# Optimization experiments

Hardware: AMD Instinct MI355X
Metric: run time of the kernel (lower is better)

## Reference

```python
import jax, jax.numpy as jnp
import numpy as np

DIM = 128
B = 8
HM, WM = 64, 64  # target (m) spatial size


def setup_inputs() -> dict:
    key = jax.random.key(0)
    ks = jax.random.split(key, 20)
    d = DIM
    sc = 1.0 / np.sqrt(d)       # GRU / 1x1-conv fan-in scale
    sc_in = 1.0 / np.sqrt(3 * d)
    f32 = jnp.float32
    return {
        'l': jax.random.normal(ks[0], (B, d, 2 * HM, 2 * WM), f32),
        'm': jax.random.normal(ks[1], (B, d, HM, WM), f32),
        's': jax.random.normal(ks[2], (B, d, HM // 2, WM // 2), f32),
        'proj_in_w': jax.random.normal(ks[3], (d, 3 * d), f32) * sc_in,
        'proj_in_scale': jax.random.uniform(ks[4], (d,), f32, 0.5, 1.5),
        'proj_in_shift': jax.random.normal(ks[5], (d,), f32) * 0.1,
        'wih_h': jax.random.normal(ks[6], (3 * d, d), f32) * sc,
        'whh_h': jax.random.normal(ks[7], (3 * d, d), f32) * sc,
        'bih_h': jax.random.normal(ks[8], (3 * d,), f32) * 0.05,
        'bhh_h': jax.random.normal(ks[9], (3 * d,), f32) * 0.05,
        'wih_w': jax.random.normal(ks[10], (3 * d, d), f32) * sc,
        'whh_w': jax.random.normal(ks[11], (3 * d, d), f32) * sc,
        'bih_w': jax.random.normal(ks[12], (3 * d,), f32) * 0.05,
        'bhh_w': jax.random.normal(ks[13], (3 * d,), f32) * 0.05,
        'gate_w': jax.random.normal(ks[14], (d, d), f32) * sc,
        'gate_b': jax.random.normal(ks[15], (d,), f32) * 0.05,
        'proj_out_w': jax.random.normal(ks[16], (d, d), f32) * sc,
        'proj_out_scale': jax.random.uniform(ks[17], (d,), f32, 0.5, 1.5),
        'proj_out_shift': jax.random.normal(ks[18], (d,), f32) * 0.1,
    }


def _conv_bn_relu(x, w, scale, shift):
    # 1x1 conv (no bias) + folded BatchNorm (per-channel affine) + ReLU
    y = jnp.einsum('bchw,oc->bohw', x, w)
    return jax.nn.relu(y * scale[None, :, None, None] + shift[None, :, None, None])


def _gru_scan(x_seq, wih, whh, bih, bhh):
    # x_seq: [T, N, d]; PyTorch GRUCell gate layout: r | z | n
    T, N, _ = x_seq.shape
    d = whh.shape[1]
    gx = jnp.einsum('tnc,gc->tng', x_seq, wih) + bih  # input gates precomputed

    def step(h, gx_t):
        gh = h @ whh.T + bhh
        r = jax.nn.sigmoid(gx_t[:, :d] + gh[:, :d])
        z = jax.nn.sigmoid(gx_t[:, d:2 * d] + gh[:, d:2 * d])
        n = jnp.tanh(gx_t[:, 2 * d:] + r * gh[:, 2 * d:])
        h_new = (1.0 - z) * n + z * h
        return h_new, h_new

    h0 = jnp.zeros((N, d), x_seq.dtype)
    _, out = jax.lax.scan(step, h0, gx)
    return out  # [T, N, d]


def _forward(l, m, s, proj_in_w, proj_in_scale, proj_in_shift,
             wih_h, whh_h, bih_h, bhh_h, wih_w, whh_w, bih_w, bhh_w,
             gate_w, gate_b, proj_out_w, proj_out_scale, proj_out_shift):
    b, _, H, W = m.shape
    lr = jax.image.resize(l, (b, l.shape[1], H, W), 'bilinear')  # align_corners=False
    sr = jax.image.resize(s, (b, s.shape[1], H, W), 'bilinear')
    x = _conv_bn_relu(jnp.concatenate([lr, m, sr], axis=1),
                      proj_in_w, proj_in_scale, proj_in_shift)  # [b,c,H,W]
    c = x.shape[1]

    # vertical scan: sequence over H, batch (b, W)
    xh = jnp.transpose(x, (2, 0, 3, 1)).reshape(H, b * W, c)
    oh = _gru_scan(xh, wih_h, whh_h, bih_h, bhh_h).reshape(H, b, W, c)
    oh = jnp.transpose(oh, (1, 3, 0, 2))  # [b,c,H,W]

    # horizontal scan: sequence over W, batch (b, H)
    xw = jnp.transpose(x, (3, 0, 2, 1)).reshape(W, b * H, c)
    ow = _gru_scan(xw, wih_w, whh_w, bih_w, bhh_w).reshape(W, b, H, c)
    ow = jnp.transpose(ow, (1, 3, 2, 0))  # [b,c,H,W]

    scanned = oh + ow
    gate = jax.nn.sigmoid(jnp.einsum('bchw,oc->bohw', scanned, gate_w)
                          + gate_b[None, :, None, None])
    gated = scanned * gate
    return _conv_bn_relu(gated, proj_out_w, proj_out_scale, proj_out_shift) + x


def reference(l, m, s, proj_in_w, proj_in_scale, proj_in_shift,
              wih_h, whh_h, bih_h, bhh_h, wih_w, whh_w, bih_w, bhh_w,
              gate_w, gate_b, proj_out_w, proj_out_scale, proj_out_shift):
    return _forward(l, m, s, proj_in_w, proj_in_scale, proj_in_shift,
                    wih_h, whh_h, bih_h, bhh_h, wih_w, whh_w, bih_w, bhh_w,
                    gate_w, gate_b, proj_out_w, proj_out_scale, proj_out_shift)
```

## Files before the change

kernel.cpp:

```cpp
#include <hip/hip_runtime.h>


typedef __bf16 bf16;
typedef _Float16 f16;
typedef __attribute__((ext_vector_type(8))) __bf16 bf16x8;
typedef __attribute__((ext_vector_type(4))) __bf16 bf16x4;
typedef __attribute__((ext_vector_type(4))) _Float16 f16x4;
typedef __attribute__((ext_vector_type(4))) float f32x4;

__device__ __forceinline__ f32x4 mfma16(bf16x8 a, bf16x8 b, f32x4 c) {
  return __builtin_amdgcn_mfma_f32_16x16x32_bf16(a, b, c, 0, 0, 0);
}
__device__ __forceinline__ float sigm(float x) { return 1.0f / (1.0f + __expf(-x)); }
__device__ __forceinline__ float tanh_fast(float x) {
  float e = __expf(2.0f * x);
  return 1.0f - 2.0f / (e + 1.0f);
}

__global__ __launch_bounds__(256) void k_prep(
    const float* __restrict__ wpi, const float* __restrict__ wihh,
    const float* __restrict__ whhh, const float* __restrict__ wihw,
    const float* __restrict__ whhw, const float* __restrict__ wg,
    const float* __restrict__ wpo, bf16* __restrict__ dst) {
  int i = blockIdx.x * 256 + threadIdx.x;
  if (i < 49152) dst[i] = (bf16)wpi[i];
  else if (i < 98304) dst[i] = (bf16)wihh[i - 49152];
  else if (i < 147456) dst[i] = (bf16)whhh[i - 98304];
  else if (i < 196608) dst[i] = (bf16)wihw[i - 147456];
  else if (i < 245760) dst[i] = (bf16)whhw[i - 196608];
  else if (i < 262144) dst[i] = (bf16)wg[i - 245760];
  else if (i < 278528) dst[i] = (bf16)wpo[i - 262144];
}

__global__ __launch_bounds__(256, 2) void k_projin(
    const float* __restrict__ lp, const float* __restrict__ mp,
    const float* __restrict__ sp, const float* __restrict__ pscale,
    const float* __restrict__ pshift, const bf16* __restrict__ Wpi,
    f16* __restrict__ xf16, bf16* __restrict__ xb, bf16* __restrict__ xbT) {
  __shared__ __align__(16) bf16 xin[64][392];
  const int tid = threadIdx.x;
  const int bb = blockIdx.x >> 6;
  const int h = blockIdx.x & 63;

  {
    const int wq = tid & 63, cq = tid >> 6;
    float wy[4]; int iy[4];
    {
      float ssum = 0.f;
#pragma unroll
      for (int dy = 0; dy < 4; ++dy) {
        int y = 2 * h - 1 + dy;
        bool ok = (y >= 0) && (y < 128);
        iy[dy] = ok ? y : 0;
        float w0 = (dy == 0 || dy == 3) ? 0.125f : 0.375f;
        wy[dy] = ok ? w0 : 0.f;
        ssum += wy[dy];
      }
      float inv = 1.f / ssum;
#pragma unroll
      for (int dy = 0; dy < 4; ++dy) wy[dy] *= inv;
    }
    float wx[4]; int ix[4];
    {
      float ssum = 0.f;
#pragma unroll
      for (int dx = 0; dx < 4; ++dx) {
        int xq = 2 * wq - 1 + dx;
        bool ok = (xq >= 0) && (xq < 128);
        ix[dx] = ok ? xq : 0;
        float w0 = (dx == 0 || dx == 3) ? 0.125f : 0.375f;
        wx[dx] = ok ? w0 : 0.f;
        ssum += wx[dx];
      }
      float inv = 1.f / ssum;
#pragma unroll
      for (int dx = 0; dx < 4; ++dx) wx[dx] *= inv;
    }
    int syA, syB; float wsyA, wsyB;
    {
      int j0 = (h - 1) >> 1;
      float f = (h & 1) ? 0.25f : 0.75f;
      float a = 1.f - f, b2 = f;
      if (j0 < 0) a = 0.f;
      if (j0 + 1 > 31) b2 = 0.f;
      float inv = 1.f / (a + b2);
      wsyA = a * inv; wsyB = b2 * inv;
      syA = j0 < 0 ? 0 : j0;
      syB = (j0 + 1 > 31) ? 31 : (j0 + 1);
    }
    int sxA, sxB; float wsxA, wsxB;
    {
      int j0 = (wq - 1) >> 1;
      float f = (wq & 1) ? 0.25f : 0.75f;
      float a = 1.f - f, b2 = f;
      if (j0 < 0) a = 0.f;
      if (j0 + 1 > 31) b2 = 0.f;
      float inv = 1.f / (a + b2);
      wsxA = a * inv; wsxB = b2 * inv;
      sxA = j0 < 0 ? 0 : j0;
      sxB = (j0 + 1 > 31) ? 31 : (j0 + 1);
    }
    for (int ci = 0; ci < 32; ++ci) {
      int c = cq * 32 + ci;
      const float* lc = lp + ((size_t)(bb * 128 + c) << 14);
      float acc = 0.f;
#pragma unroll
      for (int dy = 0; dy < 4; ++dy) {
        const float* row = lc + (iy[dy] << 7);
        float rs = wx[0] * row[ix[0]] + wx[1] * row[ix[1]] +
                   wx[2] * row[ix[2]] + wx[3] * row[ix[3]];
        acc = fmaf(wy[dy], rs, acc);
      }
      xin[wq][c] = (bf16)acc;
      xin[wq][128 + c] = (bf16)mp[((bb * 128 + c) * 64 + h) * 64 + wq];
      const float* sc = sp + ((size_t)(bb * 128 + c) << 10);
      float sv = wsyA * (wsxA * sc[(syA << 5) + sxA] + wsxB * sc[(syA << 5) + sxB]) +
                 wsyB * (wsxA * sc[(syB << 5) + sxA] + wsxB * sc[(syB << 5) + sxB]);
      xin[wq][256 + c] = (bf16)sv;
    }
  }
  __syncthreads();

  const int lane = tid & 63, wv = tid >> 6;
  const int l16 = lane & 15, k8 = (lane >> 4) * 8, j4 = (lane >> 4) * 4;
  const f32x4 zf = {0.f, 0.f, 0.f, 0.f};
  f32x4 acc[2][4];
#pragma unroll
  for (int i = 0; i < 2; ++i)
#pragma unroll
    for (int pt = 0; pt < 4; ++pt) acc[i][pt] = zf;

  for (int kk = 0; kk < 12; ++kk) {
    bf16x8 bfr[4];
#pragma unroll
    for (int pt = 0; pt < 4; ++pt)
      bfr[pt] = *(const bf16x8*)&xin[pt * 16 + l16][kk * 32 + k8];
#pragma unroll
    for (int i = 0; i < 2; ++i) {
      bf16x8 afr = *(const bf16x8*)(Wpi + (size_t)((wv * 2 + i) * 16 + l16) * 384 + kk * 32 + k8);
#pragma unroll
      for (int pt = 0; pt < 4; ++pt) acc[i][pt] = mfma16(afr, bfr[pt], acc[i][pt]);
    }
  }
#pragma unroll
  for (int i = 0; i < 2; ++i) {
    int c0 = (wv * 2 + i) * 16 + j4;
    f32x4 scv = *(const f32x4*)&pscale[c0];
    f32x4 shv = *(const f32x4*)&pshift[c0];
#pragma unroll
    for (int pt = 0; pt < 4; ++pt) {
      int pw = pt * 16 + l16;
      bf16x4 pk;
      f16x4 pf;
#pragma unroll
      for (int j = 0; j < 4; ++j) {
        float v = fmaxf(acc[i][pt][j] * scv[j] + shv[j], 0.f);
        xf16[(size_t)((bb * 128 + c0 + j) * 64 + h) * 64 + pw] = (f16)v;
        pk[j] = (bf16)v;
        pf[j] = (f16)v;
      }
      *(bf16x4*)&xb[(size_t)(bb * 4096 + h * 64 + pw) * 128 + c0] = pk;
      *(bf16x4*)&xbT[(size_t)(bb * 4096 + pw * 64 + h) * 128 + c0] = pk;
    }
  }
}

__global__ __launch_bounds__(512, 2) void k_gx(
    const bf16* __restrict__ xb, const bf16* __restrict__ xbT,
    const bf16* __restrict__ wih_h_b, const bf16* __restrict__ wih_w_b,
    const float* __restrict__ bih_h, const float* __restrict__ bih_w,
    const float* __restrict__ bhh_h, const float* __restrict__ bhh_w,
    f16* __restrict__ gxh, f16* __restrict__ gxw) {
  const int dir = blockIdx.z;
  const int nb = blockIdx.y;
  const int t0 = blockIdx.x * 2;
  const bf16* xsrc = dir ? xbT : xb;
  const bf16* wih = dir ? wih_w_b : wih_h_b;
  const float* bih = dir ? bih_w : bih_h;
  const float* bhh = dir ? bhh_w : bhh_h;
  f16* gx = dir ? gxw : gxh;

  const int tid = threadIdx.x, lane = tid & 63, w = tid >> 6;
  const int l16 = lane & 15, k8 = (lane >> 4) * 8, j4 = (lane >> 4) * 4;
  const int n = nb * 16 + l16;
  const int pb = n >> 6, q = n & 63;

  bf16x8 afr[3][4];
#pragma unroll
  for (int part = 0; part < 3; ++part) {
    int gbase = part * 128 + w * 16;
#pragma unroll
    for (int kk = 0; kk < 4; ++kk)
      afr[part][kk] = *(const bf16x8*)(wih + (size_t)(gbase + l16) * 128 + kk * 32 + k8);
  }
  const f32x4 zf = {0.f, 0.f, 0.f, 0.f};
  f32x4 acc[3][2];
#pragma unroll
  for (int part = 0; part < 3; ++part) { acc[part][0] = zf; acc[part][1] = zf; }

#pragma unroll
  for (int pt = 0; pt < 2; ++pt) {
    const bf16* xr = xsrc + (size_t)(pb * 4096 + (t0 + pt) * 64 + q) * 128;
#pragma unroll
    for (int kk = 0; kk < 4; ++kk) {
      bf16x8 bfr = *(const bf16x8*)(xr + kk * 32 + k8);
#pragma unroll
      for (int part = 0; part < 3; ++part)
        acc[part][pt] = mfma16(afr[part][kk], bfr, acc[part][pt]);
    }
  }
#pragma unroll
  for (int part = 0; part < 3; ++part) {
    int g0 = part * 128 + w * 16 + j4;
    f32x4 bi = *(const f32x4*)&bih[g0];
    if (part < 2) {
      f32x4 bh = *(const f32x4*)&bhh[g0];
#pragma unroll
      for (int j = 0; j < 4; ++j) bi[j] += bh[j];
    }
#pragma unroll
    for (int pt = 0; pt < 2; ++pt) {
      f16x4 pk;
#pragma unroll
      for (int j = 0; j < 4; ++j) pk[j] = (f16)(acc[part][pt][j] + bi[j]);
      *(f16x4*)&gx[((size_t)(((t0 + pt) * 32 + nb) * 3 + part) * 512 + tid) * 4] = pk;
    }
  }
}

__global__ __launch_bounds__(512, 2) void k_scan(
    const bf16* __restrict__ whh_h_b, const bf16* __restrict__ whh_w_b,
    const float* __restrict__ bhh_h, const float* __restrict__ bhh_w,
    const f16* __restrict__ gxh, const f16* __restrict__ gxw,
    f16* __restrict__ ohb, f16* __restrict__ owb) {
  const int dir = blockIdx.x >> 5;
  const int nb = blockIdx.x & 31;
  const int nbase = nb * 16;
  const bf16* whh = dir ? whh_w_b : whh_h_b;
  const float* bhh = dir ? bhh_w : bhh_h;
  const f16* gx = dir ? gxw : gxh;
  f16* outb = dir ? owb : ohb;

  __shared__ __align__(16) bf16 hbuf[2][16][136];

  const int tid = threadIdx.x, lane = tid & 63, w = tid >> 6;
  const int l16 = lane & 15, k8 = (lane >> 4) * 8, j4 = (lane >> 4) * 4;
  const int cc0 = w * 16 + j4;

  bf16x8 afr[3][4];
#pragma unroll
  for (int part = 0; part < 3; ++part) {
    int gbase = part * 128 + w * 16;
#pragma unroll
    for (int kk = 0; kk < 4; ++kk)
      afr[part][kk] = *(const bf16x8*)(whh + (size_t)(gbase + l16) * 128 + kk * 32 + k8);
  }
  const f32x4 bhn = *(const f32x4*)&bhh[256 + cc0];

  for (int i = tid; i < 2 * 16 * 136; i += 512) ((bf16*)hbuf)[i] = (bf16)0.f;

  const int n = nbase + l16;
  const int pb = n >> 6, q = n & 63;
  const int pbase0 = pb * 4096 + (dir ? q * 64 : q);
  const int pstep = dir ? 1 : 64;

  f16x4 gxr, gxz, gxn;
  {
    const size_t b0 = ((size_t)(0 * 32 + nb) * 3) * 512 + tid;
    gxr = *(const f16x4*)&gx[(b0) * 4];
    gxz = *(const f16x4*)&gx[(b0 + 512) * 4];
    gxn = *(const f16x4*)&gx[(b0 + 1024) * 4];
  }
  f32x4 hreg = {0.f, 0.f, 0.f, 0.f};
  int cur = 0;
  __syncthreads();

  const f32x4 zf = {0.f, 0.f, 0.f, 0.f};
  for (int t = 0; t < 64; ++t) {
    bf16x8 hb[4];
#pragma unroll
    for (int kk = 0; kk < 4; ++kk)
      hb[kk] = *(const bf16x8*)&hbuf[cur][l16][kk * 32 + k8];
    f16x4 gxr_n, gxz_n, gxn_n;
    {
      int tn = t < 63 ? t + 1 : 63;
      const size_t b0 = ((size_t)(tn * 32 + nb) * 3) * 512 + tid;
      gxr_n = *(const f16x4*)&gx[(b0) * 4];
      gxz_n = *(const f16x4*)&gx[(b0 + 512) * 4];
      gxn_n = *(const f16x4*)&gx[(b0 + 1024) * 4];
    }
    f32x4 aR = zf, aZ = zf, aN = zf;
#pragma unroll
    for (int kk = 0; kk < 4; ++kk) {
      aR = mfma16(afr[0][kk], hb[kk], aR);
      aZ = mfma16(afr[1][kk], hb[kk], aZ);
      aN = mfma16(afr[2][kk], hb[kk], aN);
    }
    bf16x4 hb4;
    f16x4 o4;
#pragma unroll
    for (int j = 0; j < 4; ++j) {
      float r = sigm((float)gxr[j] + aR[j]);
      float z = sigm((float)gxz[j] + aZ[j]);
      float nn = tanh_fast((float)gxn[j] + r * (aN[j] + bhn[j]));
      float h = nn + z * (hreg[j] - nn);
      hreg[j] = h;
      hb4[j] = (bf16)h;
      o4[j] = (f16)h;
    }
    *(bf16x4*)&hbuf[cur ^ 1][l16][cc0] = hb4;
    *(f16x4*)&outb[(size_t)(pbase0 + t * pstep) * 128 + cc0] = o4;
    __syncthreads();
    cur ^= 1;
    gxr = gxr_n; gxz = gxz_n; gxn = gxn_n;
  }
}

__global__ __launch_bounds__(256, 2) void k_final(
    const f16* __restrict__ ohb, const f16* __restrict__ owb,
    const bf16* __restrict__ Wg, const float* __restrict__ gate_b,
    const bf16* __restrict__ Wpo, const float* __restrict__ poscale,
    const float* __restrict__ poshift, const f16* __restrict__ xf16,
    float* __restrict__ out) {
  __shared__ __align__(16) float sf[64][132];
  __shared__ __align__(16) bf16 sb[64][136];
  __shared__ __align__(16) bf16 gbuf[64][136];
  const int tid = threadIdx.x;
  const int bb = blockIdx.x >> 6, h = blockIdx.x & 63;
  const int pbase = bb * 4096 + h * 64;
  for (int i = tid; i < 8192; i += 256) {
    int w = i >> 7, cc = i & 127;
    size_t idx = (size_t)(pbase + w) * 128 + cc;
    float v = (float)ohb[idx] + (float)owb[idx];
    sf[w][cc] = v;
    sb[w][cc] = (bf16)v;
  }
  __syncthreads();
  const int lane = tid & 63, wv = tid >> 6;
  const int l16 = lane & 15, k8 = (lane >> 4) * 8, j4 = (lane >> 4) * 4;
  const f32x4 zf = {0.f, 0.f, 0.f, 0.f};
  f32x4 acc[2][4];
#pragma unroll
  for (int i = 0; i < 2; ++i)
#pragma unroll
    for (int pt = 0; pt < 4; ++pt) acc[i][pt] = zf;
#pragma unroll
  for (int kk = 0; kk < 4; ++kk) {
    bf16x8 bfr[4];
#pragma unroll
    for (int pt = 0; pt < 4; ++pt)
      bfr[pt] = *(const bf16x8*)&sb[pt * 16 + l16][kk * 32 + k8];
#pragma unroll
    for (int i = 0; i < 2; ++i) {
      bf16x8 afr = *(const bf16x8*)(Wg + (size_t)((wv * 2 + i) * 16 + l16) * 128 + kk * 32 + k8);
#pragma unroll
      for (int pt = 0; pt < 4; ++pt) acc[i][pt] = mfma16(afr, bfr[pt], acc[i][pt]);
    }
  }
#pragma unroll
  for (int i = 0; i < 2; ++i) {
    int o0 = (wv * 2 + i) * 16 + j4;
    f32x4 gb4 = *(const f32x4*)&gate_b[o0];
#pragma unroll
    for (int pt = 0; pt < 4; ++pt) {
      int pc = pt * 16 + l16;
      f32x4 sv = *(const f32x4*)&sf[pc][o0];
      bf16x4 pk;
#pragma unroll
      for (int j = 0; j < 4; ++j) {
        float g = sigm(acc[i][pt][j] + gb4[j]);
        pk[j] = (bf16)(sv[j] * g);
      }
      *(bf16x4*)&gbuf[pc][o0] = pk;
    }
  }
  __syncthreads();
  f32x4 acc2[2][4];
#pragma unroll
  for (int i = 0; i < 2; ++i)
#pragma unroll
    for (int pt = 0; pt < 4; ++pt) acc2[i][pt] = zf;
#pragma unroll
  for (int kk = 0; kk < 4; ++kk) {
    bf16x8 bfr[4];
#pragma unroll
    for (int pt = 0; pt < 4; ++pt)
      bfr[pt] = *(const bf16x8*)&gbuf[pt * 16 + l16][kk * 32 + k8];
#pragma unroll
    for (int i = 0; i < 2; ++i) {
      bf16x8 afr = *(const bf16x8*)(Wpo + (size_t)((wv * 2 + i) * 16 + l16) * 128 + kk * 32 + k8);
#pragma unroll
      for (int pt = 0; pt < 4; ++pt) acc2[i][pt] = mfma16(afr, bfr[pt], acc2[i][pt]);
    }
  }
#pragma unroll
  for (int i = 0; i < 2; ++i) {
    int o0 = (wv * 2 + i) * 16 + j4;
    f32x4 scv = *(const f32x4*)&poscale[o0];
    f32x4 shv = *(const f32x4*)&poshift[o0];
#pragma unroll
    for (int pt = 0; pt < 4; ++pt) {
      int pc = pt * 16 + l16;
#pragma unroll
      for (int j = 0; j < 4; ++j) {
        int oc = o0 + j;
        size_t oi = (size_t)((bb * 128 + oc) * 64 + h) * 64 + pc;
        float v = fmaxf(acc2[i][pt][j] * scv[j] + shv[j], 0.f) + (float)xf16[oi];
        out[oi] = v;
      }
    }
  }
}

extern "C" void kernel_launch(void* const* d_in, const int* in_sizes, int n_in,
                              void* d_out, int out_size, void* d_ws, size_t ws_size,
                              hipStream_t stream) {
  const float* lp = (const float*)d_in[0];
  const float* mp = (const float*)d_in[1];
  const float* sp = (const float*)d_in[2];
  const float* proj_in_w = (const float*)d_in[3];
  const float* proj_in_scale = (const float*)d_in[4];
  const float* proj_in_shift = (const float*)d_in[5];
  const float* wih_h = (const float*)d_in[6];
  const float* whh_h = (const float*)d_in[7];
  const float* bih_h = (const float*)d_in[8];
  const float* bhh_h = (const float*)d_in[9];
  const float* wih_w = (const float*)d_in[10];
  const float* whh_w = (const float*)d_in[11];
  const float* bih_w = (const float*)d_in[12];
  const float* bhh_w = (const float*)d_in[13];
  const float* gate_w = (const float*)d_in[14];
  const float* gate_b = (const float*)d_in[15];
  const float* proj_out_w = (const float*)d_in[16];
  const float* proj_out_scale = (const float*)d_in[17];
  const float* proj_out_shift = (const float*)d_in[18];
  float* out = (float*)d_out;

  char* ws = (char*)d_ws;
  bf16* wb = (bf16*)ws;
  bf16* Wpi_b = wb + 0;
  bf16* Wih_h_b = wb + 49152;
  bf16* Whh_h_b = wb + 98304;
  bf16* Wih_w_b = wb + 147456;
  bf16* Whh_w_b = wb + 196608;
  bf16* Wg_b = wb + 245760;
  bf16* Wpo_b = wb + 262144;
  f16* xf16 = (f16*)(ws + 557056);
  bf16* xb = (bf16*)(ws + 8945664);
  bf16* xbT = (bf16*)(ws + 17334272);
  f16* gxh = (f16*)(ws + 25722880);
  f16* gxw = (f16*)(ws + 50888704);
  f16* ohb = (f16*)(ws + 76054528);
  f16* owb = (f16*)(ws + 84443136);

  k_prep<<<dim3(1088), dim3(256), 0, stream>>>(proj_in_w, wih_h, whh_h, wih_w,
                                               whh_w, gate_w, proj_out_w, wb);
  k_projin<<<dim3(512), dim3(256), 0, stream>>>(lp, mp, sp, proj_in_scale,
                                                proj_in_shift, Wpi_b, xf16, xb, xbT);
  k_gx<<<dim3(32, 32, 2), dim3(512), 0, stream>>>(xb, xbT, Wih_h_b, Wih_w_b,
                                                  bih_h, bih_w, bhh_h, bhh_w,
                                                  gxh, gxw);
  k_scan<<<dim3(64), dim3(512), 0, stream>>>(Whh_h_b, Whh_w_b, bhh_h, bhh_w,
                                             gxh, gxw, ohb, owb);
  k_final<<<dim3(512), dim3(256), 0, stream>>>(ohb, owb, Wg_b, gate_b, Wpo_b,
                                               proj_out_scale, proj_out_shift,
                                               xf16, out);
}
```

Before: 309.2 us.

## Double projin threads, shuffle-based downsample loads, and lighter scan barrier

k_projin now runs 512 threads per block, so each wave computes one 16-channel output tile and each thread stages 16 input channels instead of 32. The 4-tap horizontal downsample of l now uses one vectorized float2 load plus lane shuffles in place of four scattered loads. In k_scan, the gx prefetch is issued before the LDS hidden-state read, and __syncthreads is replaced by an explicit lgkmcnt wait plus s_barrier, which skips waiting on outstanding global stores. The shuffle trick relies on adjacent lanes holding adjacent output columns. The hand-written barrier depends on the compiler not needing the vmcnt wait that __syncthreads would normally emit.

```diff
diff --git a/kernel.cpp b/kernel.cpp
--- a/kernel.cpp
+++ b/kernel.cpp
@@ -7,6 +7,7 @@
 typedef __attribute__((ext_vector_type(4))) __bf16 bf16x4;
 typedef __attribute__((ext_vector_type(4))) _Float16 f16x4;
 typedef __attribute__((ext_vector_type(4))) float f32x4;
+typedef __attribute__((ext_vector_type(2))) float f32x2;
 
 __device__ __forceinline__ f32x4 mfma16(bf16x8 a, bf16x8 b, f32x4 c) {
   return __builtin_amdgcn_mfma_f32_16x16x32_bf16(a, b, c, 0, 0, 0);
@@ -32,7 +33,7 @@
   else if (i < 278528) dst[i] = (bf16)wpo[i - 262144];
 }
 
-__global__ __launch_bounds__(256, 2) void k_projin(
+__global__ __launch_bounds__(512, 2) void k_projin(
     const float* __restrict__ lp, const float* __restrict__ mp,
     const float* __restrict__ sp, const float* __restrict__ pscale,
     const float* __restrict__ pshift, const bf16* __restrict__ Wpi,
@@ -60,14 +61,13 @@
 #pragma unroll
       for (int dy = 0; dy < 4; ++dy) wy[dy] *= inv;
     }
-    float wx[4]; int ix[4];
+    float wx[4];
     {
       float ssum = 0.f;
 #pragma unroll
       for (int dx = 0; dx < 4; ++dx) {
         int xq = 2 * wq - 1 + dx;
         bool ok = (xq >= 0) && (xq < 128);
-        ix[dx] = ok ? xq : 0;
         float w0 = (dx == 0 || dx == 3) ? 0.125f : 0.375f;
         wx[dx] = ok ? w0 : 0.f;
         ssum += wx[dx];
@@ -100,15 +100,18 @@
       sxA = j0 < 0 ? 0 : j0;
       sxB = (j0 + 1 > 31) ? 31 : (j0 + 1);
     }
-    for (int ci = 0; ci < 32; ++ci) {
-      int c = cq * 32 + ci;
+#pragma unroll 4
+    for (int ci = 0; ci < 16; ++ci) {
+      int c = cq * 16 + ci;
       const float* lc = lp + ((size_t)(bb * 128 + c) << 14);
       float acc = 0.f;
 #pragma unroll
       for (int dy = 0; dy < 4; ++dy) {
         const float* row = lc + (iy[dy] << 7);
-        float rs = wx[0] * row[ix[0]] + wx[1] * row[ix[1]] +
-                   wx[2] * row[ix[2]] + wx[3] * row[ix[3]];
+        f32x2 v = *(const f32x2*)&row[2 * wq];
+        float bprev = __shfl_up(v.y, 1);
+        float anext = __shfl_down(v.x, 1);
+        float rs = wx[0] * bprev + wx[1] * v.x + wx[2] * v.y + wx[3] * anext;
         acc = fmaf(wy[dy], rs, acc);
       }
       xin[wq][c] = (bf16)acc;
@@ -124,40 +127,32 @@
   const int lane = tid & 63, wv = tid >> 6;
   const int l16 = lane & 15, k8 = (lane >> 4) * 8, j4 = (lane >> 4) * 4;
   const f32x4 zf = {0.f, 0.f, 0.f, 0.f};
-  f32x4 acc[2][4];
-#pragma unroll
-  for (int i = 0; i < 2; ++i)
-#pragma unroll
-    for (int pt = 0; pt < 4; ++pt) acc[i][pt] = zf;
+  f32x4 acc[4];
+#pragma unroll
+  for (int pt = 0; pt < 4; ++pt) acc[pt] = zf;
 
   for (int kk = 0; kk < 12; ++kk) {
     bf16x8 bfr[4];
 #pragma unroll
     for (int pt = 0; pt < 4; ++pt)
       bfr[pt] = *(const bf16x8*)&xin[pt * 16 + l16][kk * 32 + k8];
-#pragma unroll
-    for (int i = 0; i < 2; ++i) {
-      bf16x8 afr = *(const bf16x8*)(Wpi + (size_t)((wv * 2 + i) * 16 + l16) * 384 + kk * 32 + k8);
-#pragma unroll
-      for (int pt = 0; pt < 4; ++pt) acc[i][pt] = mfma16(afr, bfr[pt], acc[i][pt]);
-    }
-  }
-#pragma unroll
-  for (int i = 0; i < 2; ++i) {
-    int c0 = (wv * 2 + i) * 16 + j4;
+    bf16x8 afr = *(const bf16x8*)(Wpi + (size_t)(wv * 16 + l16) * 384 + kk * 32 + k8);
+#pragma unroll
+    for (int pt = 0; pt < 4; ++pt) acc[pt] = mfma16(afr, bfr[pt], acc[pt]);
+  }
+  {
+    int c0 = wv * 16 + j4;
     f32x4 scv = *(const f32x4*)&pscale[c0];
     f32x4 shv = *(const f32x4*)&pshift[c0];
 #pragma unroll
     for (int pt = 0; pt < 4; ++pt) {
       int pw = pt * 16 + l16;
       bf16x4 pk;
-      f16x4 pf;
 #pragma unroll
       for (int j = 0; j < 4; ++j) {
-        float v = fmaxf(acc[i][pt][j] * scv[j] + shv[j], 0.f);
+        float v = fmaxf(acc[pt][j] * scv[j] + shv[j], 0.f);
         xf16[(size_t)((bb * 128 + c0 + j) * 64 + h) * 64 + pw] = (f16)v;
         pk[j] = (bf16)v;
-        pf[j] = (f16)v;
       }
       *(bf16x4*)&xb[(size_t)(bb * 4096 + h * 64 + pw) * 128 + c0] = pk;
       *(bf16x4*)&xbT[(size_t)(bb * 4096 + pw * 64 + h) * 128 + c0] = pk;
@@ -235,7 +230,6 @@
     f16* __restrict__ ohb, f16* __restrict__ owb) {
   const int dir = blockIdx.x >> 5;
   const int nb = blockIdx.x & 31;
-  const int nbase = nb * 16;
   const bf16* whh = dir ? whh_w_b : whh_h_b;
   const float* bhh = dir ? bhh_w : bhh_h;
   const f16* gx = dir ? gxw : gxh;
@@ -259,14 +253,14 @@
 
   for (int i = tid; i < 2 * 16 * 136; i += 512) ((bf16*)hbuf)[i] = (bf16)0.f;
 
-  const int n = nbase + l16;
+  const int n = nb * 16 + l16;
   const int pb = n >> 6, q = n & 63;
   const int pbase0 = pb * 4096 + (dir ? q * 64 : q);
   const int pstep = dir ? 1 : 64;
 
   f16x4 gxr, gxz, gxn;
   {
-    const size_t b0 = ((size_t)(0 * 32 + nb) * 3) * 512 + tid;
+    const size_t b0 = ((size_t)nb * 3) * 512 + tid;
     gxr = *(const f16x4*)&gx[(b0) * 4];
     gxz = *(const f16x4*)&gx[(b0 + 512) * 4];
     gxn = *(const f16x4*)&gx[(b0 + 1024) * 4];
@@ -277,10 +271,6 @@
 
   const f32x4 zf = {0.f, 0.f, 0.f, 0.f};
   for (int t = 0; t < 64; ++t) {
-    bf16x8 hb[4];
-#pragma unroll
-    for (int kk = 0; kk < 4; ++kk)
-      hb[kk] = *(const bf16x8*)&hbuf[cur][l16][kk * 32 + k8];
     f16x4 gxr_n, gxz_n, gxn_n;
     {
       int tn = t < 63 ? t + 1 : 63;
@@ -289,6 +279,10 @@
       gxz_n = *(const f16x4*)&gx[(b0 + 512) * 4];
       gxn_n = *(const f16x4*)&gx[(b0 + 1024) * 4];
     }
+    bf16x8 hb[4];
+#pragma unroll
+    for (int kk = 0; kk < 4; ++kk)
+      hb[kk] = *(const bf16x8*)&hbuf[cur][l16][kk * 32 + k8];
     f32x4 aR = zf, aZ = zf, aN = zf;
 #pragma unroll
     for (int kk = 0; kk < 4; ++kk) {
@@ -310,7 +304,7 @@
     }
     *(bf16x4*)&hbuf[cur ^ 1][l16][cc0] = hb4;
     *(f16x4*)&outb[(size_t)(pbase0 + t * pstep) * 128 + cc0] = o4;
-    __syncthreads();
+    asm volatile("s_waitcnt lgkmcnt(0)\n\ts_barrier" ::: "memory");
     cur ^= 1;
     gxr = gxr_n; gxz = gxz_n; gxn = gxn_n;
   }
@@ -455,7 +449,7 @@
 
   k_prep<<<dim3(1088), dim3(256), 0, stream>>>(proj_in_w, wih_h, whh_h, wih_w,
                                                whh_w, gate_w, proj_out_w, wb);
-  k_projin<<<dim3(512), dim3(256), 0, stream>>>(lp, mp, sp, proj_in_scale,
+  k_projin<<<dim3(512), dim3(512), 0, stream>>>(lp, mp, sp, proj_in_scale,
                                                 proj_in_shift, Wpi_b, xf16, xb, xbT);
   k_gx<<<dim3(32, 32, 2), dim3(512), 0, stream>>>(xb, xbT, Wih_h_b, Wih_w_b,
                                                   bih_h, bih_w, bhh_h, bhh_w,
```

New measurement: 293.0 us. 5.3% less time.
